# Performance work log

Hardware: AMD Instinct MI355X
Metric: run time of the kernel (lower is better)

Reference implementation:

```python
import jax, jax.numpy as jnp
import numpy as np

SPATIAL_SHAPES = [(128, 128), (64, 64), (32, 32), (16, 16)]  # sum HW = 21760
N_HEADS, N_LEVELS, N_POINTS, EMBED = 8, 4, 4, 256
HEAD_D = EMBED // N_HEADS
B, NQ = 2, 10000
NV = sum(h * w for h, w in SPATIAL_SHAPES)


def setup_inputs() -> dict:
    key = jax.random.key(0)
    ks = jax.random.split(key, 12)
    s = 0.02
    return {
        "query": jax.random.normal(ks[0], (B, NQ, EMBED), jnp.float32),
        "key": jax.random.normal(ks[1], (B, NV, EMBED), jnp.float32),
        "value": jax.random.normal(ks[2], (B, NV, EMBED), jnp.float32),
        "W_off": jax.random.normal(ks[3], (EMBED, N_HEADS * N_LEVELS * N_POINTS * 2), jnp.float32) * s,
        "b_off": jax.random.uniform(ks[4], (N_HEADS * N_LEVELS * N_POINTS * 2,), jnp.float32, -0.9, 0.9),
        "W_attn": jax.random.normal(ks[5], (EMBED, N_HEADS * N_LEVELS * N_POINTS), jnp.float32) * s,
        "b_attn": jnp.zeros((N_HEADS * N_LEVELS * N_POINTS,), jnp.float32),
        "W_v": jax.random.normal(ks[6], (EMBED, EMBED), jnp.float32) * s,
        "b_v": jnp.zeros((EMBED,), jnp.float32),
        "W_out": jax.random.normal(ks[7], (EMBED, EMBED), jnp.float32) * s,
        "b_out": jnp.zeros((EMBED,), jnp.float32),
    }


def bilinear_sample(img, gx, gy):
    """img: [N, Hs, Ws, C]; gx, gy: [N, P] in [-1, 1].
    Torch grid_sample semantics: bilinear, align_corners=True, padding_mode='zeros'.
    gx indexes width, gy indexes height."""
    N, Hs, Ws, C = img.shape
    px = (gx + 1.0) * 0.5 * (Ws - 1)
    py = (gy + 1.0) * 0.5 * (Hs - 1)
    x0 = jnp.floor(px)
    y0 = jnp.floor(py)
    wx = (px - x0)[..., None]
    wy = (py - y0)[..., None]
    x0i = x0.astype(jnp.int32)
    y0i = y0.astype(jnp.int32)
    flat = img.reshape(N, Hs * Ws, C)

    def gather(xi, yi):
        valid = ((xi >= 0) & (xi < Ws) & (yi >= 0) & (yi < Hs))[..., None]
        xc = jnp.clip(xi, 0, Ws - 1)
        yc = jnp.clip(yi, 0, Hs - 1)
        idx = yc * Ws + xc  # [N, P]
        v = jnp.take_along_axis(flat, idx[..., None], axis=1)  # [N, P, C]
        return jnp.where(valid, v, 0.0)

    v00 = gather(x0i, y0i)
    v01 = gather(x0i + 1, y0i)
    v10 = gather(x0i, y0i + 1)
    v11 = gather(x0i + 1, y0i + 1)
    top = v00 * (1.0 - wx) + v01 * wx
    bot = v10 * (1.0 - wx) + v11 * wx
    return top * (1.0 - wy) + bot * wy


def reference(query, key, value, W_off, b_off, W_attn, b_attn, W_v, b_v, W_out, b_out):
    Bq, Nq, _ = query.shape
    # value projection -> per-head values
    v = (value @ W_v + b_v).reshape(Bq, NV, N_HEADS, HEAD_D)
    # sampling locations (used directly as normalized [-1,1] grid coords) and weights
    off = (query @ W_off + b_off).reshape(Bq, Nq, N_HEADS, N_LEVELS, N_POINTS, 2)
    attn = (query @ W_attn + b_attn).reshape(Bq, Nq, N_HEADS, N_LEVELS, N_POINTS)
    attn = jax.nn.softmax(attn, axis=-1)  # softmax over points per level (as in source)

    out = jnp.zeros((Bq, Nq, EMBED), query.dtype)
    start = 0
    for lvl, (Hs, Ws) in enumerate(SPATIAL_SHAPES):
        vl = v[:, start:start + Hs * Ws].reshape(Bq, Hs, Ws, N_HEADS, HEAD_D)
        start += Hs * Ws
        vl = vl.transpose(0, 3, 1, 2, 4).reshape(Bq * N_HEADS, Hs, Ws, HEAD_D)
        gl = off[:, :, :, lvl]  # [B, Nq, H, P, 2]
        gl = gl.transpose(0, 2, 1, 3, 4).reshape(Bq * N_HEADS, Nq * N_POINTS, 2)
        samp = bilinear_sample(vl, gl[..., 0], gl[..., 1])  # [B*H, Nq*P, D]
        samp = samp.reshape(Bq, N_HEADS, Nq, N_POINTS, HEAD_D)
        wl = attn[:, :, :, lvl].transpose(0, 2, 1, 3)  # [B, H, Nq, P]
        out = out + jnp.einsum('bhqp,bhqpd->bqhd', wl, samp).reshape(Bq, Nq, EMBED)
    return out @ W_out + b_out
```

## Files before the change

### kernel.cpp

```cpp
#include <hip/hip_runtime.h>
#include <math.h>

#define B_   2
#define NQ_  10000
#define NV_  21760
#define EMB  256
#define MQ   (B_*NQ_)
#define MV   (B_*NV_)

typedef short bf16x8 __attribute__((ext_vector_type(8)));
typedef float f32x4  __attribute__((ext_vector_type(4)));

__device__ constexpr int LSc[4] = {0, 16384, 20480, 21504};

__device__ __forceinline__ unsigned short f2bf(float x) {
  unsigned u = __builtin_bit_cast(unsigned, x);
  u += 0x7FFFu + ((u >> 16) & 1u);
  return (unsigned short)(u >> 16);
}
__device__ __forceinline__ float bf2f(unsigned short s) {
  return __builtin_bit_cast(float, (unsigned)s << 16);
}

__global__ __launch_bounds__(256) void prep_weights(
    const float* __restrict__ Wv, const float* __restrict__ Wattn,
    const float* __restrict__ Woff, const float* __restrict__ Wout,
    unsigned short* __restrict__ WvT, unsigned short* __restrict__ WoutT,
    unsigned short* __restrict__ WqHi, unsigned short* __restrict__ WqLo) {
  int n = blockIdx.x;
  int k = threadIdx.x;
  if (n < 256) {
    WvT[n * 256 + k] = f2bf(Wv[k * 256 + n]);
  } else if (n < 512) {
    int c = n - 256;
    WoutT[c * 256 + k] = f2bf(Wout[k * 256 + c]);
  } else {
    int qr = n - 512;
    float x = (qr < 256) ? Woff[k * 256 + qr] : Wattn[k * 128 + (qr - 256)];
    unsigned short hi = f2bf(x);
    WqHi[qr * 256 + k] = hi;
    WqLo[qr * 256 + k] = f2bf(x - bf2f(hi));
  }
}

template <int MODE, typename OutT, bool VPERM = false>
__global__ __launch_bounds__(256) void gemm_mfma(
    const void* __restrict__ Aa,
    const unsigned short* __restrict__ Bt, const unsigned short* __restrict__ Bt2,
    const float* __restrict__ bias, const float* __restrict__ bias2,
    OutT* __restrict__ C, float* __restrict__ C2, int M, int N) {
  constexpr int BM = 128, BK = 32;
  __shared__ unsigned short As[(MODE == 3 ? 2 : 1) * BM * BK];
  __shared__ unsigned short Bs[(MODE == 3 ? 2 : 1) * BM * BK];
  unsigned short* As2 = As + BM * BK;
  unsigned short* Bs2 = Bs + BM * BK;

  const int tid = threadIdx.x;
  const int lane = tid & 63, wv = tid >> 6;
  const int wr = wv >> 1, wc = wv & 1;
  const int row0 = blockIdx.x * BM, col0 = blockIdx.y * BM;

  auto lds_addr = [](int row, int kslot) -> int {
    return row * 64 + ((kslot ^ ((row >> 1) & 3)) << 4);
  };

  auto stage_bf = [&](unsigned short* dst, const unsigned short* src,
                      int rbase, int rmax, int kk) {
#pragma unroll
    for (int i = 0; i < 2; ++i) {
      int idx = tid + 256 * i;
      int row = idx >> 2, ks = idx & 3;
      int rg = min(rbase + row, rmax);
      int xorb = (row >> 1) & 3;
      const unsigned short* gp =
          src + (size_t)rg * 256 + kk + ((ks ^ xorb) << 3);
      unsigned short* lp = dst + (size_t)(wv * 64 + i * 256) * 8;
      __builtin_amdgcn_global_load_lds(
          (const __attribute__((address_space(1))) void*)gp,
          (__attribute__((address_space(3))) void*)lp, 16, 0, 0);
    }
  };
  auto stage_cvt = [&](unsigned short* dst, const float* src,
                       int rbase, int rmax, int kk) {
#pragma unroll
    for (int i = 0; i < 4; ++i) {
      int idx = tid + 256 * i;
      int row = idx >> 3, c4 = idx & 7;
      int rg = min(rbase + row, rmax);
      float4 vdat = *(const float4*)(src + (size_t)rg * 256 + kk + c4 * 4);
      ushort4 o;
      o.x = f2bf(vdat.x); o.y = f2bf(vdat.y);
      o.z = f2bf(vdat.z); o.w = f2bf(vdat.w);
      *(ushort4*)((char*)dst + lds_addr(row, c4 >> 1) + (c4 & 1) * 8) = o;
    }
  };
  auto stage_cvt2 = [&](unsigned short* dstH, unsigned short* dstL,
                        const float* src, int rbase, int rmax, int kk) {
#pragma unroll
    for (int i = 0; i < 4; ++i) {
      int idx = tid + 256 * i;
      int row = idx >> 3, c4 = idx & 7;
      int rg = min(rbase + row, rmax);
      float4 vdat = *(const float4*)(src + (size_t)rg * 256 + kk + c4 * 4);
      ushort4 hh, ll;
      hh.x = f2bf(vdat.x); ll.x = f2bf(vdat.x - bf2f(hh.x));
      hh.y = f2bf(vdat.y); ll.y = f2bf(vdat.y - bf2f(hh.y));
      hh.z = f2bf(vdat.z); ll.z = f2bf(vdat.z - bf2f(hh.z));
      hh.w = f2bf(vdat.w); ll.w = f2bf(vdat.w - bf2f(hh.w));
      int a = lds_addr(row, c4 >> 1) + (c4 & 1) * 8;
      *(ushort4*)((char*)dstH + a) = hh;
      *(ushort4*)((char*)dstL + a) = ll;
    }
  };

  const bool three_term = (MODE == 3) && (col0 < 256);

  f32x4 acc[4][4] = {};

  for (int kk = 0; kk < 256; kk += BK) {
    if (kk) __syncthreads();
    if constexpr (MODE == 1)
      stage_cvt(As, (const float*)Aa, row0, M - 1, kk);
    else if constexpr (MODE == 3) {
      if (three_term)
        stage_cvt2(As, As2, (const float*)Aa, row0, M - 1, kk);
      else
        stage_cvt(As, (const float*)Aa, row0, M - 1, kk);
    } else
      stage_bf(As, (const unsigned short*)Aa, row0, M - 1, kk);
    stage_bf(Bs, Bt, col0, N - 1, kk);
    if constexpr (MODE == 3)
      if (three_term) stage_bf(Bs2, Bt2, col0, N - 1, kk);
    __syncthreads();

    const int kslot = lane >> 4;
    bf16x8 af[4], bfr[4];
#pragma unroll
    for (int i = 0; i < 4; ++i) {
      int ra = wr * 64 + i * 16 + (lane & 15);
      af[i] = *(const bf16x8*)((const char*)As + lds_addr(ra, kslot));
      int rb = wc * 64 + i * 16 + (lane & 15);
      bfr[i] = *(const bf16x8*)((const char*)Bs + lds_addr(rb, kslot));
    }
#pragma unroll
    for (int mi = 0; mi < 4; ++mi)
#pragma unroll
      for (int ni = 0; ni < 4; ++ni)
        acc[mi][ni] = __builtin_amdgcn_mfma_f32_16x16x32_bf16(
            af[mi], bfr[ni], acc[mi][ni], 0, 0, 0);

    if constexpr (MODE == 3) {
      if (three_term) {
        bf16x8 af2[4], bfr2[4];
#pragma unroll
        for (int i = 0; i < 4; ++i) {
          int ra = wr * 64 + i * 16 + (lane & 15);
          af2[i] = *(const bf16x8*)((const char*)As2 + lds_addr(ra, kslot));
          int rb = wc * 64 + i * 16 + (lane & 15);
          bfr2[i] = *(const bf16x8*)((const char*)Bs2 + lds_addr(rb, kslot));
        }
#pragma unroll
        for (int mi = 0; mi < 4; ++mi)
#pragma unroll
          for (int ni = 0; ni < 4; ++ni) {
            acc[mi][ni] = __builtin_amdgcn_mfma_f32_16x16x32_bf16(
                af2[mi], bfr[ni], acc[mi][ni], 0, 0, 0);
            acc[mi][ni] = __builtin_amdgcn_mfma_f32_16x16x32_bf16(
                af[mi], bfr2[ni], acc[mi][ni], 0, 0, 0);
          }
      }
    }
  }

  if constexpr (VPERM) {
    float bb4[4];
#pragma unroll
    for (int ni = 0; ni < 4; ++ni)
      bb4[ni] = bias[col0 + wc * 64 + ni * 16 + (lane & 15)];
#pragma unroll
    for (int mi = 0; mi < 4; ++mi) {
#pragma unroll
      for (int r = 0; r < 4; ++r) {
        int row = row0 + wr * 64 + mi * 16 + ((lane >> 4) << 2) + r;
        int pix = row, bb2 = 0;
        if (pix >= NV_) { bb2 = 1; pix -= NV_; }
        int lvl = (pix >= 16384) + (pix >= 20480) + (pix >= 21504);
        int sh = 7 - lvl;
        int rel = pix - LSc[lvl];
        int x = rel & ((1 << sh) - 1), y = rel >> sh;
        unsigned pairoff = ((unsigned)((y << (sh - 1)) + (x >> 1)) << 10) |
                           ((unsigned)(x & 1) << 3);
        char* vout = (char*)C + ((size_t)bb2 * NV_ + LSc[lvl]) * 512 + pairoff;
#pragma unroll
        for (int ni = 0; ni < 4; ++ni) {
          int gcol = col0 + wc * 64 + ni * 16 + (lane & 15);
          float val = acc[mi][ni][r] + bb4[ni];
          int h = gcol >> 5, d = gcol & 31;
          *(unsigned short*)(vout + h * 128 + (d >> 2) * 16 + (d & 3) * 2) =
              f2bf(val);
        }
      }
    }
  } else {
#pragma unroll
    for (int ni = 0; ni < 4; ++ni) {
      int gcol = col0 + wc * 64 + ni * 16 + (lane & 15);
      float bb = (MODE == 3 && gcol >= 256) ? bias2[gcol - 256] : bias[gcol];
#pragma unroll
      for (int mi = 0; mi < 4; ++mi) {
        int rowbase = row0 + wr * 64 + mi * 16 + ((lane >> 4) << 2);
        f32x4 a = acc[mi][ni];
#pragma unroll
        for (int r = 0; r < 4; ++r) {
          int row = rowbase + r;
          if (row < M) {
            float val = a[r] + bb;
            if constexpr (MODE == 3) {
              if (gcol >= 256)
                C2[(size_t)row * 128 + (gcol - 256)] = val;
              else
                C[(size_t)row * 256 + gcol] = (OutT)val;
            } else if constexpr (sizeof(OutT) == 2) {
              C[(size_t)row * N + gcol] = (OutT)f2bf(val);
            } else {
              C[(size_t)row * N + gcol] = (OutT)val;
            }
          }
        }
      }
    }
  }
}

__global__ __launch_bounds__(512) void msda_sample7(
    const char* __restrict__ v,
    const float* __restrict__ off,
    const float* __restrict__ attnlg,
    ushort4* __restrict__ tmp4) {
  __shared__ unsigned coeff[4 * 136 * 8];
  const int tid = threadIdx.x;
  const int lane = tid & 63;
  const int wid = tid >> 6;
  const int wq = wid >> 1;
  const int w = wid & 1;
  const int bq = blockIdx.x * 4 + wq;
  const int b = (blockIdx.x * 4) / NQ_;

  unsigned* cbase = coeff + wq * (136 * 8);
  const float* offq = off + (size_t)bq * 256;
  const float* attq = attnlg + (size_t)bq * 128;

  {
    int h = lane >> 3, dl = (lane >> 2) & 1, p = lane & 3;
    int l = 2 * w + dl;
    int Wl = 128 >> l, sh = 7 - l;

    const float* lg = attq + h * 16 + l * 4;
    float l0 = lg[0], l1 = lg[1], l2 = lg[2], l3 = lg[3];
    float m = fmaxf(fmaxf(l0, l1), fmaxf(l2, l3));
    float e0 = expf(l0 - m), e1 = expf(l1 - m);
    float e2 = expf(l2 - m), e3 = expf(l3 - m);
    float ep = (p == 0) ? e0 : (p == 1) ? e1 : (p == 2) ? e2 : e3;
    float wsm = ep / (e0 + e1 + e2 + e3);

    float gx = offq[h * 32 + (l * 4 + p) * 2 + 0];
    float gy = offq[h * 32 + (l * 4 + p) * 2 + 1];
    float s = 0.5f * (float)(Wl - 1);
    float px = fmaf(gx, s, s), py = fmaf(gy, s, s);
    float x0f = floorf(px), y0f = floorf(py);
    float wx = px - x0f, wy = py - y0f;
    int x0 = (int)x0f, y0 = (int)y0f;

    bool bx0 = (unsigned)x0 < (unsigned)Wl, bx1 = (unsigned)(x0 + 1) < (unsigned)Wl;
    bool by0 = (unsigned)y0 < (unsigned)Wl, by1 = (unsigned)(y0 + 1) < (unsigned)Wl;
    int x0c = min(max(x0, 0), Wl - 1), x1c = min(max(x0 + 1, 0), Wl - 1);
    int y0c = min(max(y0, 0), Wl - 1), y1c = min(max(y0 + 1, 0), Wl - 1);

    auto poff = [&](int xx, int yy) -> unsigned {
      return ((unsigned)((yy << (sh - 1)) + (xx >> 1)) << 10) |
             ((unsigned)(xx & 1) << 3);
    };

    float wxm = 1.f - wx, wym = 1.f - wy;
    float w00 = (bx0 & by0) ? wsm * wxm * wym : 0.f;
    float w01 = (bx1 & by0) ? wsm * wx  * wym : 0.f;
    float w10 = (bx0 & by1) ? wsm * wxm * wy  : 0.f;
    float w11 = (bx1 & by1) ? wsm * wx  * wy  : 0.f;

    unsigned* slot = cbase + (h * 17 + l * 4 + p) * 8;
    uint4 s0;
    s0.x = poff(x0c, y0c);
    s0.y = poff(x1c, y0c);
    s0.z = poff(x0c, y1c);
    s0.w = poff(x1c, y1c);
    *(uint4*)slot = s0;
    uint4 s1;
    s1.x = __builtin_bit_cast(unsigned, w00);
    s1.y = __builtin_bit_cast(unsigned, w01);
    s1.z = __builtin_bit_cast(unsigned, w10);
    s1.w = __builtin_bit_cast(unsigned, w11);
    *(uint4*)(slot + 4) = s1;
  }
  __syncthreads();

  const int h = lane >> 3, c4 = lane & 7;
  const unsigned laneoff = (unsigned)(h * 128 + c4 * 16);
  float4 acc = make_float4(0.f, 0.f, 0.f, 0.f);

#pragma unroll
  for (int dl = 0; dl < 2; ++dl) {
    const int l = 2 * w + dl;
    const char* lb = v + ((size_t)b * NV_ + LSc[l]) * 512;
    const unsigned* cb = cbase + (h * 17 + l * 4) * 8;
#pragma unroll
    for (int p = 0; p < 4; ++p) {
      uint4 s0 = *(const uint4*)(cb + p * 8);
      uint4 s1 = *(const uint4*)(cb + p * 8 + 4);
      float w00 = __builtin_bit_cast(float, s1.x);
      float w01 = __builtin_bit_cast(float, s1.y);
      float w10 = __builtin_bit_cast(float, s1.z);
      float w11 = __builtin_bit_cast(float, s1.w);

      uint2 r00 = *(const uint2*)(lb + (laneoff + s0.x));
      uint2 r01 = *(const uint2*)(lb + (laneoff + s0.y));
      uint2 r10 = *(const uint2*)(lb + (laneoff + s0.z));
      uint2 r11 = *(const uint2*)(lb + (laneoff + s0.w));

      acc.x += w00 * __builtin_bit_cast(float, r00.x << 16)
             + w01 * __builtin_bit_cast(float, r01.x << 16)
             + w10 * __builtin_bit_cast(float, r10.x << 16)
             + w11 * __builtin_bit_cast(float, r11.x << 16);
      acc.y += w00 * __builtin_bit_cast(float, r00.x & 0xFFFF0000u)
             + w01 * __builtin_bit_cast(float, r01.x & 0xFFFF0000u)
             + w10 * __builtin_bit_cast(float, r10.x & 0xFFFF0000u)
             + w11 * __builtin_bit_cast(float, r11.x & 0xFFFF0000u);
      acc.z += w00 * __builtin_bit_cast(float, r00.y << 16)
             + w01 * __builtin_bit_cast(float, r01.y << 16)
             + w10 * __builtin_bit_cast(float, r10.y << 16)
             + w11 * __builtin_bit_cast(float, r11.y << 16);
      acc.w += w00 * __builtin_bit_cast(float, r00.y & 0xFFFF0000u)
             + w01 * __builtin_bit_cast(float, r01.y & 0xFFFF0000u)
             + w10 * __builtin_bit_cast(float, r10.y & 0xFFFF0000u)
             + w11 * __builtin_bit_cast(float, r11.y & 0xFFFF0000u);
    }
  }

  __syncthreads();
  float4* red = (float4*)coeff;
  if (w == 1) red[wq * 64 + lane] = acc;
  __syncthreads();
  if (w == 0) {
    float4 o2 = red[wq * 64 + lane];
    acc.x += o2.x; acc.y += o2.y; acc.z += o2.z; acc.w += o2.w;
    ushort4 o;
    o.x = f2bf(acc.x); o.y = f2bf(acc.y); o.z = f2bf(acc.z); o.w = f2bf(acc.w);
    tmp4[(size_t)bq * 64 + lane] = o;
  }
}

extern "C" void kernel_launch(void* const* d_in, const int* in_sizes, int n_in,
                              void* d_out, int out_size, void* d_ws, size_t ws_size,
                              hipStream_t stream) {
  const float* query  = (const float*)d_in[0];
  const float* value  = (const float*)d_in[2];
  const float* W_off  = (const float*)d_in[3];
  const float* b_off  = (const float*)d_in[4];
  const float* W_attn = (const float*)d_in[5];
  const float* b_attn = (const float*)d_in[6];
  const float* W_v    = (const float*)d_in[7];
  const float* b_v    = (const float*)d_in[8];
  const float* W_out  = (const float*)d_in[9];
  const float* b_out  = (const float*)d_in[10];
  float* out = (float*)d_out;

  char* p = (char*)d_ws;
  unsigned short* v_bf  = (unsigned short*)p; p += (size_t)MV * 256 * 2;
  float*          off_w = (float*)p;          p += (size_t)MQ * 256 * 4;
  float*          att_w = (float*)p;          p += (size_t)MQ * 128 * 4;
  unsigned short* tmp_bf= (unsigned short*)p; p += (size_t)MQ * 256 * 2;
  unsigned short* WvT   = (unsigned short*)p; p += 256 * 256 * 2;
  unsigned short* WoutT = (unsigned short*)p; p += 256 * 256 * 2;
  unsigned short* WqHi  = (unsigned short*)p; p += 384 * 256 * 2;
  unsigned short* WqLo  = (unsigned short*)p; p += 384 * 256 * 2;

  prep_weights<<<dim3(896), dim3(256), 0, stream>>>(
      W_v, W_attn, W_off, W_out, WvT, WoutT, WqHi, WqLo);

  gemm_mfma<1, unsigned short, true><<<dim3(MV / 128, 2), dim3(256), 0, stream>>>(
      value, WvT, nullptr, b_v, nullptr, v_bf, nullptr, MV, 256);

  gemm_mfma<3, float><<<dim3((MQ + 127) / 128, 3), dim3(256), 0, stream>>>(
      query, WqHi, WqLo, b_off, b_attn, off_w, att_w, MQ, 384);

  msda_sample7<<<dim3(MQ / 4), dim3(512), 0, stream>>>(
      (const char*)v_bf, off_w, att_w, (ushort4*)tmp_bf);

  gemm_mfma<0, float><<<dim3((MQ + 127) / 128, 2), dim3(256), 0, stream>>>(
      tmp_bf, WoutT, nullptr, b_out, nullptr, out, nullptr, MQ, 256);
}
```

Before: 125.3 us.

## Stage permuted value output in LDS, store attention logits as bf16, shrink sampler blocks

The value-projection epilogue now writes its permuted bf16 tile into shared memory and then copies it out with coalesced 16-byte stores, where before it issued scattered 2-byte global stores. The attention logits are stored as bf16 instead of fp32, which halves that buffer and its read traffic in the sampler. The sampling kernel also moves from 512 to 256 threads per block, handling 2 queries per block instead of 4. In exchange, the logits lose precision before the softmax, and the GEMM epilogue gains extra barriers and a larger shared-memory footprint.

```diff
diff --git a/kernel.cpp b/kernel.cpp
--- a/kernel.cpp
+++ b/kernel.cpp
@@ -48,12 +48,14 @@
     const void* __restrict__ Aa,
     const unsigned short* __restrict__ Bt, const unsigned short* __restrict__ Bt2,
     const float* __restrict__ bias, const float* __restrict__ bias2,
-    OutT* __restrict__ C, float* __restrict__ C2, int M, int N) {
+    OutT* __restrict__ C, unsigned short* __restrict__ C2, int M, int N) {
   constexpr int BM = 128, BK = 32;
-  __shared__ unsigned short As[(MODE == 3 ? 2 : 1) * BM * BK];
-  __shared__ unsigned short Bs[(MODE == 3 ? 2 : 1) * BM * BK];
-  unsigned short* As2 = As + BM * BK;
-  unsigned short* Bs2 = Bs + BM * BK;
+  constexpr int SMEM_SHORTS = (MODE == 3 || VPERM) ? 16384 : 8192;
+  __shared__ unsigned short smem[SMEM_SHORTS];
+  unsigned short* As  = smem;
+  unsigned short* Bs  = smem + ((MODE == 3) ? 2 : 1) * BM * BK;
+  unsigned short* As2 = smem + BM * BK;
+  unsigned short* Bs2 = smem + 3 * BM * BK;
 
   const int tid = threadIdx.x;
   const int lane = tid & 63, wv = tid >> 6;
@@ -177,29 +179,38 @@
 #pragma unroll
     for (int ni = 0; ni < 4; ++ni)
       bb4[ni] = bias[col0 + wc * 64 + ni * 16 + (lane & 15)];
+    __syncthreads();
+    unsigned short* pbuf = smem;
 #pragma unroll
     for (int mi = 0; mi < 4; ++mi) {
 #pragma unroll
       for (int r = 0; r < 4; ++r) {
-        int row = row0 + wr * 64 + mi * 16 + ((lane >> 4) << 2) + r;
-        int pix = row, bb2 = 0;
-        if (pix >= NV_) { bb2 = 1; pix -= NV_; }
-        int lvl = (pix >= 16384) + (pix >= 20480) + (pix >= 21504);
-        int sh = 7 - lvl;
-        int rel = pix - LSc[lvl];
-        int x = rel & ((1 << sh) - 1), y = rel >> sh;
-        unsigned pairoff = ((unsigned)((y << (sh - 1)) + (x >> 1)) << 10) |
-                           ((unsigned)(x & 1) << 3);
-        char* vout = (char*)C + ((size_t)bb2 * NV_ + LSc[lvl]) * 512 + pairoff;
+        int lr = wr * 64 + mi * 16 + ((lane >> 4) << 2) + r;
+        int pb = lr >> 1, par = lr & 1;
 #pragma unroll
         for (int ni = 0; ni < 4; ++ni) {
-          int gcol = col0 + wc * 64 + ni * 16 + (lane & 15);
+          int lc = wc * 64 + ni * 16 + (lane & 15);
           float val = acc[mi][ni][r] + bb4[ni];
-          int h = gcol >> 5, d = gcol & 31;
-          *(unsigned short*)(vout + h * 128 + (d >> 2) * 16 + (d & 3) * 2) =
-              f2bf(val);
+          int hl = lc >> 5, d = lc & 31;
+          int off = pb * 512 + hl * 128 + ((d >> 2) << 4) + (par << 3) +
+                    ((d & 3) << 1);
+          *(unsigned short*)((char*)pbuf + off) = f2bf(val);
         }
       }
+    }
+    __syncthreads();
+    int pix0 = row0, bb2 = 0;
+    if (pix0 >= NV_) { bb2 = 1; pix0 -= NV_; }
+    int lvl = (pix0 >= 16384) + (pix0 >= 20480) + (pix0 >= 21504);
+    int rel0 = pix0 - LSc[lvl];
+    char* dst = (char*)C + ((size_t)bb2 * NV_ + LSc[lvl]) * 512 +
+                (size_t)(rel0 >> 1) * 1024 + (size_t)(col0 >> 5) * 128;
+    int pb = tid >> 2, q = tid & 3;
+#pragma unroll
+    for (int i = 0; i < 8; ++i) {
+      int u = q * 16 + i * 64;
+      uint4 vd = *(const uint4*)((const char*)pbuf + pb * 512 + u);
+      *(uint4*)(dst + (size_t)pb * 1024 + u) = vd;
     }
   } else {
 #pragma unroll
@@ -217,9 +228,9 @@
             float val = a[r] + bb;
             if constexpr (MODE == 3) {
               if (gcol >= 256)
-                C2[(size_t)row * 128 + (gcol - 256)] = val;
+                C2[(size_t)row * 128 + (gcol - 256)] = f2bf(val);
               else
-                C[(size_t)row * 256 + gcol] = (OutT)val;
+                ((float*)C)[(size_t)row * 256 + gcol] = val;
             } else if constexpr (sizeof(OutT) == 2) {
               C[(size_t)row * N + gcol] = (OutT)f2bf(val);
             } else {
@@ -232,31 +243,34 @@
   }
 }
 
-__global__ __launch_bounds__(512) void msda_sample7(
+__global__ __launch_bounds__(256) void msda_sample7(
     const char* __restrict__ v,
     const float* __restrict__ off,
-    const float* __restrict__ attnlg,
+    const unsigned short* __restrict__ attnlg,
     ushort4* __restrict__ tmp4) {
-  __shared__ unsigned coeff[4 * 136 * 8];
+  __shared__ unsigned coeff[2 * 136 * 8];
   const int tid = threadIdx.x;
   const int lane = tid & 63;
   const int wid = tid >> 6;
   const int wq = wid >> 1;
   const int w = wid & 1;
-  const int bq = blockIdx.x * 4 + wq;
-  const int b = (blockIdx.x * 4) / NQ_;
+  const int bq = blockIdx.x * 2 + wq;
+  const int b = (blockIdx.x * 2) / NQ_;
 
   unsigned* cbase = coeff + wq * (136 * 8);
   const float* offq = off + (size_t)bq * 256;
-  const float* attq = attnlg + (size_t)bq * 128;
+  const unsigned short* attq = attnlg + (size_t)bq * 128;
 
   {
     int h = lane >> 3, dl = (lane >> 2) & 1, p = lane & 3;
     int l = 2 * w + dl;
     int Wl = 128 >> l, sh = 7 - l;
 
-    const float* lg = attq + h * 16 + l * 4;
-    float l0 = lg[0], l1 = lg[1], l2 = lg[2], l3 = lg[3];
+    uint2 lg = *(const uint2*)(attq + h * 16 + l * 4);
+    float l0 = __builtin_bit_cast(float, lg.x << 16);
+    float l1 = __builtin_bit_cast(float, lg.x & 0xFFFF0000u);
+    float l2 = __builtin_bit_cast(float, lg.y << 16);
+    float l3 = __builtin_bit_cast(float, lg.y & 0xFFFF0000u);
     float m = fmaxf(fmaxf(l0, l1), fmaxf(l2, l3));
     float e0 = expf(l0 - m), e1 = expf(l1 - m);
     float e2 = expf(l2 - m), e3 = expf(l3 - m);
@@ -376,7 +390,7 @@
   char* p = (char*)d_ws;
   unsigned short* v_bf  = (unsigned short*)p; p += (size_t)MV * 256 * 2;
   float*          off_w = (float*)p;          p += (size_t)MQ * 256 * 4;
-  float*          att_w = (float*)p;          p += (size_t)MQ * 128 * 4;
+  unsigned short* att_w = (unsigned short*)p; p += (size_t)MQ * 128 * 2;
   unsigned short* tmp_bf= (unsigned short*)p; p += (size_t)MQ * 256 * 2;
   unsigned short* WvT   = (unsigned short*)p; p += 256 * 256 * 2;
   unsigned short* WoutT = (unsigned short*)p; p += 256 * 256 * 2;
@@ -392,7 +406,7 @@
   gemm_mfma<3, float><<<dim3((MQ + 127) / 128, 3), dim3(256), 0, stream>>>(
       query, WqHi, WqLo, b_off, b_attn, off_w, att_w, MQ, 384);
 
-  msda_sample7<<<dim3(MQ / 4), dim3(512), 0, stream>>>(
+  msda_sample7<<<dim3(MQ / 2), dim3(256), 0, stream>>>(
       (const char*)v_bf, off_w, att_w, (ushort4*)tmp_bf);
 
   gemm_mfma<0, float><<<dim3((MQ + 127) / 128, 2), dim3(256), 0, stream>>>(
```

After: 120.2 us (median of 2 runs). -4.1%, faster.
